# Optimization experiments

Measured on AMD Instinct MI355X. Metric: run time of the kernel, lower is better.

The kernel has to match this reference:

```python
import jax, jax.numpy as jnp
import numpy as np
from jax import lax

# Module config (from init_kwargs)
PADDING = (1, 1)
DILATION = (1, 1)
GROUPS = 1
# stride param is initialized to ones(2); effective integer stride = floor(stride) = (1, 1).
# Output shape depends on this value, so it must be static under jit.
INT_STRIDE = (1, 1)


def setup_inputs() -> dict:
    key = jax.random.key(0)
    k1, k2 = jax.random.split(key)
    B, Cin, H, W = 32, 128, 64, 64
    Cout, kH, kW = 256, 3, 3
    x = jax.random.normal(k1, (B, Cin, H, W), dtype=jnp.float32)
    # reset_parameters: uniform(-stdv, stdv), stdv = 1/sqrt(Cin*kH*kW)
    stdv = 1.0 / np.sqrt(Cin * kH * kW)
    weight = jax.random.uniform(k2, (Cout, Cin // GROUPS, kH, kW), dtype=jnp.float32,
                                minval=-stdv, maxval=stdv)
    stride = jnp.ones((2,), dtype=jnp.float32)
    return {"x": x, "weight": weight, "stride": stride}


def reference(x, weight, stride):
    # Integer strides = floor(stride); with stride initialized to ones this is (1, 1).
    # (Static under jit; floor has zero derivative a.e., so stride only affects
    #  sampling locations, exactly as in the CUDA im2col forward.)
    out = lax.conv_general_dilated(
        x, weight,
        window_strides=INT_STRIDE,
        padding=[(PADDING[0], PADDING[0]), (PADDING[1], PADDING[1])],
        rhs_dilation=DILATION,
        dimension_numbers=("NCHW", "OIHW", "NCHW"),
        feature_group_count=GROUPS,
    )
    return out
```

## Files before the change

### kernel.cpp

```cpp
#include <hip/hip_runtime.h>

typedef __attribute__((ext_vector_type(8))) short short8;
typedef __attribute__((ext_vector_type(4))) float f32x4;

#define XP_ELEMS (32u * 66u * 66u * 128u)
#define WT_ELEMS (256u * 1152u)
#define WS_NEED  ((size_t)(XP_ELEMS + WT_ELEMS) * 2u)

typedef const __attribute__((address_space(1))) void* gp1_t;
typedef __attribute__((address_space(3))) void* lp3_t;

__device__ __forceinline__ void gload16(const void* g, void* l) {
  __builtin_amdgcn_global_load_lds((gp1_t)g, (lp3_t)l, 16, 0, 0);
}

__device__ __forceinline__ short f2bf(float f) {
  unsigned u = __float_as_uint(f);
  u = (u + 0x7FFFu + ((u >> 16) & 1u)) >> 16;
  return (short)u;
}

__global__ __launch_bounds__(256) void prepass_x(const float* __restrict__ x,
                                                 short* __restrict__ xp) {
  int tid  = blockIdx.x * 256 + threadIdx.x;
  int o8   = tid * 8;
  int cin0 = o8 & 127;
  int pix  = o8 >> 7;
  int px   = pix % 66;
  int t2   = pix / 66;
  int py   = t2 % 66;
  int b    = t2 / 66;
  short8 v;
  if (px == 0 || px == 65 || py == 0 || py == 65) {
    v = (short8)0;
  } else {
    const float* src = x + (((long)(b * 128 + cin0) * 64 + (py - 1)) * 64 + (px - 1));
#pragma unroll
    for (int i = 0; i < 8; ++i) v[i] = f2bf(src[(long)i * 4096]);
  }
  *(short8*)(xp + o8) = v;
}

__global__ __launch_bounds__(256) void prepass_w(const float* __restrict__ w,
                                                 short* __restrict__ wt) {
  int o    = blockIdx.x * 256 + threadIdx.x;
  int cout = o / 1152;
  int r    = o % 1152;
  int kh   = r / 384;
  int kw   = (r / 128) % 3;
  int cin  = r & 127;
  wt[o] = f2bf(w[((cout * 128 + cin) * 3 + kh) * 3 + kw]);
}

__global__ __launch_bounds__(256) void conv_gemm(const short* __restrict__ xp,
                                                 const short* __restrict__ wt,
                                                 float* __restrict__ out) {
  __shared__ short Alds[128 * 32];
  __shared__ short Blds[128 * 32];
  const int tid   = threadIdx.x;
  const int w     = tid >> 6;
  const int l     = tid & 63;
  const int l15   = l & 15;
  const int q     = l >> 4;
  const int ntile = blockIdx.x;
  const int m0    = blockIdx.y << 7;

  const int srow = (w << 4) + (l >> 2);
  const int sch8 = (l & 3) * 8;

  const long aoff0 = (long)(m0 + srow) * 1152 + sch8;
  const long aoff1 = aoff0 + (long)64 * 1152;

  long boff[2];
#pragma unroll
  for (int c = 0; c < 2; ++c) {
    int ng = (ntile << 7) + (c << 6) + srow;
    int b = ng >> 12, yx = ng & 4095;
    int y = yx >> 6, xx = yx & 63;
    boff[c] = ((long)(b * 66 + y) * 66 + xx) * 128 + sch8;
  }

  short* Adst0 = &Alds[(w << 4) * 32];
  short* Adst1 = Adst0 + 64 * 32;
  short* Bdst0 = &Blds[(w << 4) * 32];
  short* Bdst1 = Bdst0 + 64 * 32;

  f32x4 acc[4][4];
#pragma unroll
  for (int i = 0; i < 4; ++i)
#pragma unroll
    for (int j = 0; j < 4; ++j) acc[i][j] = (f32x4)0.f;

  const int wm = (w >> 1) << 6;
  const int wn = (w & 1) << 6;

#pragma unroll
  for (int khkw = 0; khkw < 9; ++khkw) {
    const int kh = khkw / 3, kw = khkw % 3;
    const long sB = (long)(kh * 66 + kw) * 128;
    const int kkb = khkw << 7;
#pragma unroll
    for (int c4 = 0; c4 < 4; ++c4) {
      const int cin0 = c4 << 5;
      const int kk0  = kkb + cin0;
      gload16(wt + aoff0 + kk0, Adst0);
      gload16(wt + aoff1 + kk0, Adst1);
      gload16(xp + boff[0] + sB + cin0, Bdst0);
      gload16(xp + boff[1] + sB + cin0, Bdst1);
      __syncthreads();
      short8 af[4], bf[4];
#pragma unroll
      for (int i = 0; i < 4; ++i)
        af[i] = *(const short8*)&Alds[(wm + (i << 4) + l15) * 32 + q * 8];
#pragma unroll
      for (int j = 0; j < 4; ++j)
        bf[j] = *(const short8*)&Blds[(wn + (j << 4) + l15) * 32 + q * 8];
#pragma unroll
      for (int i = 0; i < 4; ++i)
#pragma unroll
        for (int j = 0; j < 4; ++j)
          acc[i][j] = __builtin_amdgcn_mfma_f32_16x16x32_bf16(af[i], bf[j],
                                                              acc[i][j], 0, 0, 0);
      __syncthreads();
    }
  }

  const int ngb = (ntile << 7) + wn;
  const int b   = ngb >> 12;
  const int yxb = ngb & 4095;
  float* outb = out + (long)b * (256 * 4096) + yxb + l15;
#pragma unroll
  for (int i = 0; i < 4; ++i) {
#pragma unroll
    for (int r = 0; r < 4; ++r) {
      const int cout = m0 + wm + (i << 4) + q * 4 + r;
      float* orow = outb + (long)cout * 4096;
#pragma unroll
      for (int j = 0; j < 4; ++j) orow[j * 16] = acc[i][j][r];
    }
  }
}

__global__ __launch_bounds__(256) void naive_conv(const float* __restrict__ x,
                                                  const float* __restrict__ wgt,
                                                  float* __restrict__ out) {
  long o = (long)blockIdx.x * 256 + threadIdx.x;
  int xx = (int)(o & 63);
  int y  = (int)((o >> 6) & 63);
  int co = (int)((o >> 12) & 255);
  int b  = (int)(o >> 20);
  float s = 0.f;
  for (int ci = 0; ci < 128; ++ci) {
    for (int kh = 0; kh < 3; ++kh) {
      int iy = y + kh - 1;
      if (iy < 0 || iy > 63) continue;
      for (int kw = 0; kw < 3; ++kw) {
        int ix = xx + kw - 1;
        if (ix < 0 || ix > 63) continue;
        s += x[((long)(b * 128 + ci) * 64 + iy) * 64 + ix] *
             wgt[((co * 128 + ci) * 3 + kh) * 3 + kw];
      }
    }
  }
  out[o] = s;
}

extern "C" void kernel_launch(void* const* d_in, const int* in_sizes, int n_in,
                              void* d_out, int out_size, void* d_ws, size_t ws_size,
                              hipStream_t stream) {
  (void)in_sizes; (void)n_in;
  const float* x   = (const float*)d_in[0];
  const float* wgt = (const float*)d_in[1];
  float* out = (float*)d_out;
  if (ws_size >= WS_NEED) {
    short* xp = (short*)d_ws;
    short* wt = xp + XP_ELEMS;
    prepass_x<<<dim3(XP_ELEMS / (256 * 8)), dim3(256), 0, stream>>>(x, xp);
    prepass_w<<<dim3(WT_ELEMS / 256), dim3(256), 0, stream>>>(wgt, wt);
    conv_gemm<<<dim3(1024, 2), dim3(256), 0, stream>>>(xp, wt, out);
  } else {
    naive_conv<<<dim3(out_size / 256), dim3(256), 0, stream>>>(x, wgt, out);
  }
}
```

Baseline: 288.0 us.

## Transpose input via swizzled LDS in prepass and XOR-swizzle GEMM LDS tiles

The input prepass now gives each block one (batch, row) pair. It reads coalesced float4 rows, transposes them into NHWC bf16 through a swizzled LDS buffer, and writes 16-byte vectors. The padding border is zeroed by a few threads. The GEMM kernel applies an XOR swizzle to the 16-byte chunk index when loading A and B tiles into LDS and when reading fragments back, which is meant to reduce LDS bank conflicts on the MFMA operand reads. The aim is to remove strided uncoalesced global reads in the prepass and bank conflicts in the main loop.

Measured after the change: 274.3 us. -4.8%, faster.

```diff
diff --git a/kernel.cpp b/kernel.cpp
--- a/kernel.cpp
+++ b/kernel.cpp
@@ -22,23 +22,50 @@
 
 __global__ __launch_bounds__(256) void prepass_x(const float* __restrict__ x,
                                                  short* __restrict__ xp) {
-  int tid  = blockIdx.x * 256 + threadIdx.x;
-  int o8   = tid * 8;
-  int cin0 = o8 & 127;
-  int pix  = o8 >> 7;
-  int px   = pix % 66;
-  int t2   = pix / 66;
-  int py   = t2 % 66;
-  int b    = t2 / 66;
-  short8 v;
-  if (px == 0 || px == 65 || py == 0 || py == 65) {
-    v = (short8)0;
-  } else {
-    const float* src = x + (((long)(b * 128 + cin0) * 64 + (py - 1)) * 64 + (px - 1));
-#pragma unroll
-    for (int i = 0; i < 8; ++i) v[i] = f2bf(src[(long)i * 4096]);
-  }
-  *(short8*)(xp + o8) = v;
+  __shared__ short lds[64 * 128];
+  const int y = blockIdx.x;
+  const int b = blockIdx.y;
+  const int t = threadIdx.x;
+
+  const float* src = x + (long)b * 128 * 4096 + y * 64;
+#pragma unroll
+  for (int i = 0; i < 8; ++i) {
+    int f4 = t + i * 256;
+    int cin = f4 >> 4, px4 = f4 & 15;
+    float4 v = *(const float4*)(src + (long)cin * 4096 + px4 * 4);
+    float vv[4] = {v.x, v.y, v.z, v.w};
+#pragma unroll
+    for (int j = 0; j < 4; ++j) {
+      int px = px4 * 4 + j;
+      int g = (cin >> 3) ^ ((px ^ (px >> 2)) & 15);
+      lds[px * 128 + (g << 3) + (cin & 7)] = f2bf(vv[j]);
+    }
+  }
+  __syncthreads();
+  short* dst = xp + ((long)(b * 66 + y + 1) * 66 + 1) * 128;
+#pragma unroll
+  for (int i = 0; i < 4; ++i) {
+    int f8 = t + i * 256;
+    int px = f8 >> 4, c8 = f8 & 15;
+    int g = c8 ^ ((px ^ (px >> 2)) & 15);
+    short8 v = *(const short8*)&lds[px * 128 + (g << 3)];
+    *(short8*)(dst + (long)px * 128 + c8 * 8) = v;
+  }
+  short8 z = (short8)0;
+  short* rowbase = xp + (long)(b * 66 + y + 1) * 66 * 128;
+  if (t < 32) {
+    int px = (t < 16) ? 0 : 65;
+    int c8 = t & 15;
+    *(short8*)(rowbase + (long)px * 128 + c8 * 8) = z;
+  }
+  if (y == 0) {
+    short* r0 = xp + (long)(b * 66) * 66 * 128;
+    for (int idx = t; idx < 66 * 16; idx += 256) *(short8*)(r0 + idx * 8) = z;
+  }
+  if (y == 63) {
+    short* r65 = xp + ((long)(b * 66) + 65) * 66 * 128;
+    for (int idx = t; idx < 66 * 16; idx += 256) *(short8*)(r65 + idx * 8) = z;
+  }
 }
 
 __global__ __launch_bounds__(256) void prepass_w(const float* __restrict__ w,
@@ -66,7 +93,7 @@
   const int m0    = blockIdx.y << 7;
 
   const int srow = (w << 4) + (l >> 2);
-  const int sch8 = (l & 3) * 8;
+  const int sch8 = (((l & 3) ^ ((srow >> 1) & 3)) * 8);
 
   const long aoff0 = (long)(m0 + srow) * 1152 + sch8;
   const long aoff1 = aoff0 + (long)64 * 1152;
@@ -110,11 +137,15 @@
       __syncthreads();
       short8 af[4], bf[4];
 #pragma unroll
-      for (int i = 0; i < 4; ++i)
-        af[i] = *(const short8*)&Alds[(wm + (i << 4) + l15) * 32 + q * 8];
-#pragma unroll
-      for (int j = 0; j < 4; ++j)
-        bf[j] = *(const short8*)&Blds[(wn + (j << 4) + l15) * 32 + q * 8];
+      for (int i = 0; i < 4; ++i) {
+        int rA = wm + (i << 4) + l15;
+        af[i] = *(const short8*)&Alds[rA * 32 + ((q ^ ((rA >> 1) & 3)) << 3)];
+      }
+#pragma unroll
+      for (int j = 0; j < 4; ++j) {
+        int rB = wn + (j << 4) + l15;
+        bf[j] = *(const short8*)&Blds[rB * 32 + ((q ^ ((rB >> 1) & 3)) << 3)];
+      }
 #pragma unroll
       for (int i = 0; i < 4; ++i)
 #pragma unroll
@@ -175,7 +206,7 @@
   if (ws_size >= WS_NEED) {
     short* xp = (short*)d_ws;
     short* wt = xp + XP_ELEMS;
-    prepass_x<<<dim3(XP_ELEMS / (256 * 8)), dim3(256), 0, stream>>>(x, xp);
+    prepass_x<<<dim3(64, 32), dim3(256), 0, stream>>>(x, xp);
     prepass_w<<<dim3(WT_ELEMS / 256), dim3(256), 0, stream>>>(wgt, wt);
     conv_gemm<<<dim3(1024, 2), dim3(256), 0, stream>>>(xp, wt, out);
   } else {
```
